# Kernel optimization log

Hardware: AMD Instinct MI355X
Metric: run time of the kernel (lower is better)

Reference implementation:

```python
import jax, jax.numpy as jnp
import numpy as np

N = 100000
DIM = 128
E_A = 500000
E_D = 500000


def setup_inputs() -> dict:
    key = jax.random.key(0)
    ks = jax.random.split(key, 8)
    h = jax.random.normal(ks[0], (N, DIM), dtype=jnp.float32)
    a_idx = jax.random.randint(ks[1], (E_A, 3), 0, N, dtype=jnp.int64 if jax.config.jax_enable_x64 else jnp.int32)
    a_val = jax.random.uniform(ks[2], (E_A, 1), dtype=jnp.float32)
    d_idx = jax.random.randint(ks[3], (E_D, 4), 0, N, dtype=jnp.int64 if jax.config.jax_enable_x64 else jnp.int32)
    d_val = jax.random.uniform(ks[4], (E_D, 1), dtype=jnp.float32)
    # Linear weights stored as [in, out]; init ~ Kaiming-uniform-ish scale
    W_a = jax.random.normal(ks[5], (3 * DIM + 1, DIM), dtype=jnp.float32) * (1.0 / np.sqrt(3 * DIM + 1))
    b_a = jnp.zeros((DIM,), dtype=jnp.float32)
    W_d = jax.random.normal(ks[6], (4 * DIM + 1, DIM), dtype=jnp.float32) * (1.0 / np.sqrt(4 * DIM + 1))
    b_d = jnp.zeros((DIM,), dtype=jnp.float32)
    W_h = jax.random.normal(ks[7], (3 * DIM, DIM), dtype=jnp.float32) * (1.0 / np.sqrt(3 * DIM))
    b_h = jnp.zeros((DIM,), dtype=jnp.float32)
    return {"h": h, "a_idx": a_idx, "a_val": a_val, "d_idx": d_idx, "d_val": d_val,
            "W_a": W_a, "b_a": b_a, "W_d": W_d, "b_d": b_d, "W_h": W_h, "b_h": b_h}


def reference(h, a_idx, a_val, d_idx, d_val, W_a, b_a, W_d, b_d, W_h, b_h):
    n = h.shape[0]
    # angle messages: gather 3 node embeddings + scalar, Linear + SiLU, scatter to center node
    x_a = jnp.concatenate([h[a_idx[:, 0]], h[a_idx[:, 1]], h[a_idx[:, 2]], a_val], axis=-1)  # [E_a, 3d+1]
    m_ijk = jax.nn.silu(x_a @ W_a + b_a)  # [E_a, d]
    agg_a = jax.ops.segment_sum(m_ijk, a_idx[:, 1], num_segments=n)  # [N, d]
    # dihedral messages: gather 4 node embeddings + scalar
    x_d = jnp.concatenate([h[d_idx[:, 0]], h[d_idx[:, 1]], h[d_idx[:, 2]], h[d_idx[:, 3]], d_val], axis=-1)  # [E_d, 4d+1]
    m_ijkl = jax.nn.silu(x_d @ W_d + b_d)  # [E_d, d]
    agg_d = jax.ops.segment_sum(m_ijkl, d_idx[:, 1], num_segments=n)  # [N, d]
    # residual node update
    return h + jnp.concatenate([h, agg_a, agg_d], axis=-1) @ W_h + b_h
```

## Files before the change

kernel.cpp:

```cpp
#include <hip/hip_runtime.h>
#include <hip/hip_bf16.h>

#define DIM 128
#define LDS_STRIDE 136
#define SC_STRIDE 132

typedef __attribute__((ext_vector_type(8))) __bf16 bf16x8;
typedef __attribute__((ext_vector_type(4))) __bf16 bf16x4;
typedef __attribute__((ext_vector_type(4))) float f32x4;


__global__ __launch_bounds__(256) void prep_w(const float* __restrict__ W_a,
                                              const float* __restrict__ W_d,
                                              const float* __restrict__ W_h,
                                              __bf16* __restrict__ Wt)
{
    int idx = blockIdx.x * 256 + threadIdx.x;
    if (idx >= 10 * 16384) return;
    int t   = idx >> 14;
    int rem = idx & 16383;
    int c   = rem >> 7;
    int k   = rem & 127;
    const float* src;
    if (t < 4)      src = W_d + (size_t)t * 16384;
    else if (t < 7) src = W_a + (size_t)(t - 4) * 16384;
    else            src = W_h + (size_t)(t - 7) * 16384;
    Wt[(size_t)t * 16384 + c * 128 + k] = (__bf16)src[k * 128 + c];
}

__global__ __launch_bounds__(256) void count_h2bf(const int* __restrict__ a_idx,
                                                  const int* __restrict__ d_idx,
                                                  int* __restrict__ offs,
                                                  const float* __restrict__ h,
                                                  __bf16* __restrict__ hb,
                                                  int EA, int ED, int N)
{
    const int gt = blockIdx.x * 256 + threadIdx.x;
    if (gt < EA) {
        atomicAdd(&offs[a_idx[3 * (size_t)gt + 1]], 1);
    } else if (gt < EA + ED) {
        int k = gt - EA;
        atomicAdd(&offs[N + d_idx[4 * (size_t)k + 1]], 1);
    }
    int i = gt * 8;
    if (i < N * DIM) {
        float4 v0 = *(const float4*)(h + i);
        float4 v1 = *(const float4*)(h + i + 4);
        bf16x8 o;
        o[0] = (__bf16)v0.x; o[1] = (__bf16)v0.y; o[2] = (__bf16)v0.z; o[3] = (__bf16)v0.w;
        o[4] = (__bf16)v1.x; o[5] = (__bf16)v1.y; o[6] = (__bf16)v1.z; o[7] = (__bf16)v1.w;
        *(bf16x8*)(hb + i) = o;
    }
}

__device__ __forceinline__ void stage_wt(const __bf16* __restrict__ Wtj,
                                         __bf16 (*sB)[LDS_STRIDE], int tid)
{
    for (int it = 0; it < 8; ++it) {
        int idx = tid + it * 256;
        int c  = idx >> 4;
        int k8 = (idx & 15) << 3;
        *(bf16x8*)&sB[c][k8] = *(const bf16x8*)(Wtj + c * 128 + k8);
    }
}

__device__ __forceinline__ void load_afrag_bf16(const __bf16* __restrict__ src,
                                                int row, int stride, int lk, int N,
                                                bf16x8 afrag[4])
{
    const __bf16* rp = src + (size_t)row * stride;
    #pragma unroll
    for (int ks = 0; ks < 4; ++ks) {
        bf16x8 a = {};
        if (row < N) a = *(const bf16x8*)(rp + ks * 32 + lk);
        afrag[ks] = a;
    }
}

__device__ __forceinline__ void proj_body(const __bf16* __restrict__ src,
                                          const __bf16* __restrict__ Wtj,
                                          __bf16* __restrict__ dj,
                                          __bf16 (*sB)[LDS_STRIDE],
                                          int node0, int tid, int N)
{
    float* sC = reinterpret_cast<float*>(sB);
    const int wave = tid >> 6, lane = tid & 63;
    const int lrow = lane & 15;
    const int lk   = (lane >> 4) * 8;
    const int arow = node0 + wave * 16 + lrow;

    stage_wt(Wtj, sB, tid);
    bf16x8 afrag[4];
    load_afrag_bf16(src, arow, DIM, lk, N, afrag);
    __syncthreads();

    f32x4 acc[8];
    #pragma unroll
    for (int ct = 0; ct < 8; ++ct) acc[ct] = (f32x4){0.f, 0.f, 0.f, 0.f};

    #pragma unroll
    for (int ks = 0; ks < 4; ++ks) {
        int k0 = ks * 32 + lk;
        #pragma unroll
        for (int ct = 0; ct < 8; ++ct) {
            bf16x8 b = *(const bf16x8*)&sB[ct * 16 + lrow][k0];
            acc[ct] = __builtin_amdgcn_mfma_f32_16x16x32_bf16(afrag[ks], b, acc[ct], 0, 0, 0);
        }
    }

    __syncthreads();
    {
        int rbase = wave * 16 + (lane >> 4) * 4;
        #pragma unroll
        for (int r = 0; r < 4; ++r)
            #pragma unroll
            for (int ct = 0; ct < 8; ++ct)
                sC[(rbase + r) * SC_STRIDE + ct * 16 + lrow] = acc[ct][r];
    }
    __syncthreads();

    for (int it = 0; it < 8; ++it) {
        int idx = tid + it * 256;
        int row = idx >> 5;
        int c4  = (idx & 31) << 2;
        int grow = node0 + row;
        if (grow < N) {
            const float* sp = sC + row * SC_STRIDE + c4;
            bf16x4 o;
            o[0] = (__bf16)sp[0]; o[1] = (__bf16)sp[1];
            o[2] = (__bf16)sp[2]; o[3] = (__bf16)sp[3];
            *(bf16x4*)(dj + (size_t)grow * DIM + c4) = o;
        }
    }
}

__global__ __launch_bounds__(256, 4) void projD_fill(const int* __restrict__ a_idx,
                                                     const float* __restrict__ a_val,
                                                     const int* __restrict__ d_idx,
                                                     const float* __restrict__ d_val,
                                                     int* __restrict__ offs,
                                                     int4* __restrict__ recs,
                                                     const __bf16* __restrict__ hb,
                                                     const __bf16* __restrict__ Wt,
                                                     __bf16* __restrict__ P,
                                                     int EA, int ED, int N)
{
    __shared__ __bf16 sB[128][LDS_STRIDE];
    const int tid = threadIdx.x;
    const int pb = blockIdx.x;

    int e = pb * 256 + tid;
    if (e < EA) {
        int i0 = a_idx[3 * (size_t)e + 0];
        int i1 = a_idx[3 * (size_t)e + 1];
        int i2 = a_idx[3 * (size_t)e + 2];
        int slot = atomicAdd(&offs[i1], 1);
        recs[slot] = make_int4(i0 * 256, i2 * 256, __float_as_int(a_val[e]), 0);
    } else if (e < EA + ED) {
        int k = e - EA;
        int i0 = d_idx[4 * (size_t)k + 0];
        int i1 = d_idx[4 * (size_t)k + 1];
        int i2 = d_idx[4 * (size_t)k + 2];
        int i3 = d_idx[4 * (size_t)k + 3];
        int slot = atomicAdd(&offs[N + i1], 1);
        recs[slot] = make_int4(i0 * 256, i2 * 256, i3 * 256, __float_as_int(d_val[k]));
    }

    int tile = pb >> 2, j = pb & 3;
    proj_body(hb, Wt + (size_t)j * 16384, P + (size_t)j * N * DIM,
              sB, tile * 64, tid, N);
}

__global__ __launch_bounds__(256, 4) void proj(const __bf16* __restrict__ src,
                                               const __bf16* __restrict__ Wt,
                                               __bf16* __restrict__ dst,
                                               int N)
{
    __shared__ __bf16 sB[128][LDS_STRIDE];
    const int pb = blockIdx.x;
    const int tile = pb >> 2, j = pb & 3;
    proj_body(src, Wt + (size_t)j * 16384, dst + (size_t)j * N * DIM,
              sB, tile * 64, threadIdx.x, N);
}

#define SCAN_CHUNK 1024

__global__ __launch_bounds__(256) void scan_s1(int* __restrict__ data,
                                               int* __restrict__ partials, int n)
{
    __shared__ int lds[256];
    const int t = threadIdx.x;
    const int base = blockIdx.x * SCAN_CHUNK + t * 4;
    int v[4];
    #pragma unroll
    for (int i = 0; i < 4; ++i) v[i] = (base + i < n) ? data[base + i] : 0;
    int tsum = v[0] + v[1] + v[2] + v[3];
    lds[t] = tsum; __syncthreads();
    for (int off = 1; off < 256; off <<= 1) {
        int x = (t >= off) ? lds[t - off] : 0;
        __syncthreads();
        lds[t] += x;
        __syncthreads();
    }
    if (t == 255) partials[blockIdx.x] = lds[255];
    int run = lds[t] - tsum;
    #pragma unroll
    for (int i = 0; i < 4; ++i) {
        int nv = run; run += v[i];
        if (base + i < n) data[base + i] = nv;
    }
}

__global__ __launch_bounds__(256) void scan_s2(int* __restrict__ partials, int nb)
{
    __shared__ int lds[256];
    const int t = threadIdx.x;
    int v = (t < nb) ? partials[t] : 0;
    lds[t] = v; __syncthreads();
    for (int off = 1; off < 256; off <<= 1) {
        int x = (t >= off) ? lds[t - off] : 0;
        __syncthreads();
        lds[t] += x;
        __syncthreads();
    }
    if (t < nb) partials[t] = lds[t] - v;
}

__global__ __launch_bounds__(256) void scan_s3(int* __restrict__ data,
                                               const int* __restrict__ partials, int n)
{
    const int add = partials[blockIdx.x];
    const int base = blockIdx.x * SCAN_CHUNK + threadIdx.x * 4;
    #pragma unroll
    for (int i = 0; i < 4; ++i)
        if (base + i < n) data[base + i] += add;
}

__device__ __forceinline__ float silu(float x)
{
    return x * __builtin_amdgcn_rcpf(1.f + __expf(-x));
}

__global__ __launch_bounds__(256) void gather3(const __bf16* __restrict__ P,
                                               const float* __restrict__ wlast,
                                               const float* __restrict__ bias,
                                               const int* __restrict__ offs,
                                               const int4* __restrict__ recs,
                                               __bf16* __restrict__ aggb, int N)
{
    const int tid = threadIdx.x;
    const int n = blockIdx.x * 4 + (tid >> 6);
    if (n >= N) return;
    const int lane = tid & 63;
    const int half = lane >> 5;
    const int gl = lane & 31;
    const int f  = gl * 4;
    const int fb = gl * 8;
    const size_t NBb = (size_t)N * DIM * 2;
    const char* P0b = (const char*)P;
    const char* P1b = P0b + NBb;
    const char* P2b = P0b + 2 * NBb;
    int start = (n == 0) ? 0 : offs[n - 1];
    int end = offs[n];

    float wl[4], base[4];
    {
        const float* wp = wlast + f;
        const float* bp = bias + f;
        bf16x4 p1 = *(const bf16x4*)(P1b + (size_t)n * 256 + fb);
        #pragma unroll
        for (int c = 0; c < 4; ++c) { wl[c] = wp[c]; base[c] = (float)p1[c] + bp[c]; }
    }
    float a[4] = {0.f, 0.f, 0.f, 0.f};

    const int cnt = end - start;
    const int npair = cnt >> 1;
    int s = start;
    for (int p = 0; p < npair; ++p, s += 2) {
        int4 r = recs[s + half];
        bf16x4 q0 = *(const bf16x4*)(P0b + r.x + fb);
        bf16x4 q2 = *(const bf16x4*)(P2b + r.y + fb);
        float v = __int_as_float(r.z);
        #pragma unroll
        for (int c = 0; c < 4; ++c)
            a[c] += silu((float)q0[c] + (float)q2[c] + v * wl[c] + base[c]);
    }
    if (cnt & 1) {
        int4 r = recs[end - 1];
        bf16x4 q0 = *(const bf16x4*)(P0b + r.x + fb);
        bf16x4 q2 = *(const bf16x4*)(P2b + r.y + fb);
        float v = __int_as_float(r.z);
        if (half == 0) {
            #pragma unroll
            for (int c = 0; c < 4; ++c)
                a[c] += silu((float)q0[c] + (float)q2[c] + v * wl[c] + base[c]);
        }
    }
    #pragma unroll
    for (int c = 0; c < 4; ++c) a[c] += __shfl_xor(a[c], 32, 64);
    if (half == 0) {
        bf16x4 o;
        #pragma unroll
        for (int c = 0; c < 4; ++c) o[c] = (__bf16)a[c];
        *(bf16x4*)(aggb + (size_t)n * 256 + f) = o;
    }
}

__global__ __launch_bounds__(256) void gather4(const __bf16* __restrict__ P,
                                               const float* __restrict__ wlast,
                                               const float* __restrict__ bias,
                                               const int* __restrict__ offs_d,
                                               const int4* __restrict__ recs,
                                               __bf16* __restrict__ agg, int N)
{
    const int tid = threadIdx.x;
    const int n = blockIdx.x * 4 + (tid >> 6);
    if (n >= N) return;
    const int lane = tid & 63;
    const int half = lane >> 5;
    const int gl = lane & 31;
    const int f  = gl * 4;
    const int fb = gl * 8;
    const size_t NBb = (size_t)N * DIM * 2;
    const char* P0b = (const char*)P;
    const char* P1b = P0b + NBb;
    const char* P2b = P0b + 2 * NBb;
    const char* P3b = P0b + 3 * NBb;
    int start = offs_d[n - 1];
    int end = offs_d[n];

    float wl[4], base[4];
    {
        const float* wp = wlast + f;
        const float* bp = bias + f;
        bf16x4 p1 = *(const bf16x4*)(P1b + (size_t)n * 256 + fb);
        #pragma unroll
        for (int c = 0; c < 4; ++c) { wl[c] = wp[c]; base[c] = (float)p1[c] + bp[c]; }
    }
    float a[4] = {0.f, 0.f, 0.f, 0.f};

    const int cnt = end - start;
    const int npair = cnt >> 1;
    int s = start;
    for (int p = 0; p < npair; ++p, s += 2) {
        int4 r = recs[s + half];
        bf16x4 q0 = *(const bf16x4*)(P0b + r.x + fb);
        bf16x4 q2 = *(const bf16x4*)(P2b + r.y + fb);
        bf16x4 q3 = *(const bf16x4*)(P3b + r.z + fb);
        float v = __int_as_float(r.w);
        #pragma unroll
        for (int c = 0; c < 4; ++c)
            a[c] += silu((float)q0[c] + (float)q2[c] + (float)q3[c] + v * wl[c] + base[c]);
    }
    if (cnt & 1) {
        int4 r = recs[end - 1];
        bf16x4 q0 = *(const bf16x4*)(P0b + r.x + fb);
        bf16x4 q2 = *(const bf16x4*)(P2b + r.y + fb);
        bf16x4 q3 = *(const bf16x4*)(P3b + r.z + fb);
        float v = __int_as_float(r.w);
        if (half == 0) {
            #pragma unroll
            for (int c = 0; c < 4; ++c)
                a[c] += silu((float)q0[c] + (float)q2[c] + (float)q3[c] + v * wl[c] + base[c]);
        }
    }
    #pragma unroll
    for (int c = 0; c < 4; ++c) a[c] += __shfl_xor(a[c], 32, 64);
    if (half == 0) {
        bf16x4 o;
        #pragma unroll
        for (int c = 0; c < 4; ++c) o[c] = (__bf16)a[c];
        *(bf16x4*)(agg + (size_t)n * DIM + f) = o;
    }
}

__global__ __launch_bounds__(256, 4) void update2(const float* __restrict__ h,
                                                  const __bf16* __restrict__ aggA,
                                                  const __bf16* __restrict__ aggD,
                                                  const __bf16* __restrict__ PH,
                                                  const __bf16* __restrict__ Wt,
                                                  const float* __restrict__ bh,
                                                  float* __restrict__ out, int N)
{
    __shared__ __bf16 sB[128][LDS_STRIDE];
    float* sC = reinterpret_cast<float*>(sB);
    const int tid = threadIdx.x;
    const int node0 = blockIdx.x * 64;
    const int wave = tid >> 6, lane = tid & 63;
    const int lrow = lane & 15;
    const int lk   = (lane >> 4) * 8;
    const int arow = node0 + wave * 16 + lrow;

    bf16x8 aA[4], aD[4];
    load_afrag_bf16(aggA, arow, 256, lk, N, aA);
    load_afrag_bf16(aggD, arow, DIM, lk, N, aD);

    f32x4 acc[8];
    #pragma unroll
    for (int ct = 0; ct < 8; ++ct) acc[ct] = (f32x4){0.f, 0.f, 0.f, 0.f};

    #pragma unroll
    for (int s = 0; s < 2; ++s) {
        __syncthreads();
        stage_wt(Wt + (size_t)s * 16384, sB, tid);
        __syncthreads();

        #pragma unroll
        for (int ks = 0; ks < 4; ++ks) {
            int k0 = ks * 32 + lk;
            #pragma unroll
            for (int ct = 0; ct < 8; ++ct) {
                bf16x8 b = *(const bf16x8*)&sB[ct * 16 + lrow][k0];
                bf16x8 af = (s == 0) ? aA[ks] : aD[ks];
                acc[ct] = __builtin_amdgcn_mfma_f32_16x16x32_bf16(af, b, acc[ct], 0, 0, 0);
            }
        }
    }

    __syncthreads();
    {
        int rbase = wave * 16 + (lane >> 4) * 4;
        #pragma unroll
        for (int r = 0; r < 4; ++r)
            #pragma unroll
            for (int ct = 0; ct < 8; ++ct)
                sC[(rbase + r) * SC_STRIDE + ct * 16 + lrow] = acc[ct][r];
    }
    __syncthreads();

    for (int it = 0; it < 8; ++it) {
        int idx = tid + it * 256;
        int row = idx >> 5;
        int c4  = (idx & 31) << 2;
        int grow = node0 + row;
        if (grow < N) {
            const float* sp = sC + row * SC_STRIDE + c4;
            float4 rv = *(const float4*)(h + (size_t)grow * DIM + c4);
            float4 bv = *(const float4*)(bh + c4);
            bf16x4 pv = *(const bf16x4*)(PH + (size_t)grow * DIM + c4);
            float4 ov;
            ov.x = rv.x + bv.x + (float)pv[0] + sp[0];
            ov.y = rv.y + bv.y + (float)pv[1] + sp[1];
            ov.z = rv.z + bv.z + (float)pv[2] + sp[2];
            ov.w = rv.w + bv.w + (float)pv[3] + sp[3];
            *(float4*)(out + (size_t)grow * DIM + c4) = ov;
        }
    }
}

static inline size_t align16(size_t x) { return (x + 15) & ~(size_t)15; }

extern "C" void kernel_launch(void* const* d_in, const int* in_sizes, int n_in,
                              void* d_out, int out_size, void* d_ws, size_t ws_size,
                              hipStream_t stream)
{
    const float* h     = (const float*)d_in[0];
    const int*   a_idx = (const int*)d_in[1];
    const float* a_val = (const float*)d_in[2];
    const int*   d_idx = (const int*)d_in[3];
    const float* d_val = (const float*)d_in[4];
    const float* W_a   = (const float*)d_in[5];
    const float* b_a   = (const float*)d_in[6];
    const float* W_d   = (const float*)d_in[7];
    const float* b_d   = (const float*)d_in[8];
    const float* W_h   = (const float*)d_in[9];
    const float* b_h   = (const float*)d_in[10];
    float* out = (float*)d_out;

    const int N  = in_sizes[0] / DIM;
    const int EA = in_sizes[2];
    const int ED = in_sizes[4];
    const size_t NB = (size_t)N * DIM;
    const int twoN = 2 * N;
    const int NBLK = (twoN + SCAN_CHUNK - 1) / SCAN_CHUNK;

    size_t off = 0;
    __bf16* P    = (__bf16*)((char*)d_ws + off); off = align16(off + 4 * NB * sizeof(__bf16));
    __bf16* aggD = (__bf16*)((char*)d_ws + off); off = align16(off + NB * sizeof(__bf16));
    int* offs     = (int*)((char*)d_ws + off);  off = align16(off + (size_t)twoN * sizeof(int));
    int* partials = (int*)((char*)d_ws + off);  off = align16(off + 256 * sizeof(int));
    int4* recs    = (int4*)((char*)d_ws + off); off = align16(off + (size_t)(EA + ED) * sizeof(int4));
    __bf16* Wt  = (__bf16*)((char*)d_ws + off); off = align16(off + (size_t)10 * 16384 * sizeof(__bf16));
    if (ws_size < off) return;

    const int NT64 = (N + 63) / 64;
    const int HB = (int)((NB / 8 + 255) / 256);
    const int GN4 = (N + 3) / 4;

    __bf16* h_bf = (__bf16*)d_out;
    __bf16* aggA = (__bf16*)d_out;

    prep_w<<<(10 * 16384 + 255) / 256, 256, 0, stream>>>(W_a, W_d, W_h, Wt);
    hipMemsetAsync(offs, 0, (size_t)twoN * sizeof(int), stream);

    count_h2bf<<<HB, 256, 0, stream>>>(a_idx, d_idx, offs, h, h_bf, EA, ED, N);

    scan_s1<<<NBLK, 256, 0, stream>>>(offs, partials, twoN);
    scan_s2<<<1, 256, 0, stream>>>(partials, NBLK);
    scan_s3<<<NBLK, 256, 0, stream>>>(offs, partials, twoN);

    projD_fill<<<NT64 * 4, 256, 0, stream>>>(a_idx, a_val, d_idx, d_val,
                                             offs, recs, h_bf, Wt, P, EA, ED, N);

    gather4<<<GN4, 256, 0, stream>>>(P, W_d + 512 * DIM, b_d, offs + N, recs, aggD, N);

    proj<<<NT64 * 4, 256, 0, stream>>>(h_bf, Wt + (size_t)4 * 16384, P, N);

    gather3<<<GN4, 256, 0, stream>>>(P, W_a + 384 * DIM, b_a, offs, recs, aggA, N);

    update2<<<NT64, 256, 0, stream>>>(h, aggA, aggD, P + 3 * NB, Wt + (size_t)8 * 16384,
                                      b_h, out, N);
}
```

Baseline: 319.7 us.

## Co-schedule dihedral gather with angle projection in one interleaved launch

Merges the memory-bound gather4 kernel and the MFMA-based angle projection into a single launch. Every fourth block of the first 4*NPROJ does a projection tile and the rest do gather work, so compute-heavy and latency-bound blocks share the GPU at the same time. The projection writes into a separate workspace buffer so it does not overwrite the dihedral projections gather4 is still reading. This costs extra workspace, uses the projection's LDS footprint and launch bounds for gather blocks as well, and falls back to the old sequence when the workspace is too small.

After: 380.8 us. 1.19x slower.

```diff
diff --git a/kernel.cpp b/kernel.cpp
--- a/kernel.cpp
+++ b/kernel.cpp
@@ -131,6 +131,79 @@
             o[2] = (__bf16)sp[2]; o[3] = (__bf16)sp[3];
             *(bf16x4*)(dj + (size_t)grow * DIM + c4) = o;
         }
+    }
+}
+
+__device__ __forceinline__ float silu(float x)
+{
+    return x * __builtin_amdgcn_rcpf(1.f + __expf(-x));
+}
+
+__device__ __forceinline__ void gather4_body(const __bf16* __restrict__ P,
+                                             const float* __restrict__ wlast,
+                                             const float* __restrict__ bias,
+                                             const int* __restrict__ offs_d,
+                                             const int4* __restrict__ recs,
+                                             __bf16* __restrict__ agg, int N,
+                                             int gid, int tid)
+{
+    const int n = gid * 4 + (tid >> 6);
+    if (n >= N) return;
+    const int lane = tid & 63;
+    const int half = lane >> 5;
+    const int gl = lane & 31;
+    const int f  = gl * 4;
+    const int fb = gl * 8;
+    const size_t NBb = (size_t)N * DIM * 2;
+    const char* P0b = (const char*)P;
+    const char* P1b = P0b + NBb;
+    const char* P2b = P0b + 2 * NBb;
+    const char* P3b = P0b + 3 * NBb;
+    int start = offs_d[n - 1];
+    int end = offs_d[n];
+
+    float wl[4], base[4];
+    {
+        const float* wp = wlast + f;
+        const float* bp = bias + f;
+        bf16x4 p1 = *(const bf16x4*)(P1b + (size_t)n * 256 + fb);
+        #pragma unroll
+        for (int c = 0; c < 4; ++c) { wl[c] = wp[c]; base[c] = (float)p1[c] + bp[c]; }
+    }
+    float a[4] = {0.f, 0.f, 0.f, 0.f};
+
+    const int cnt = end - start;
+    const int npair = cnt >> 1;
+    int s = start;
+    for (int p = 0; p < npair; ++p, s += 2) {
+        int4 r = recs[s + half];
+        bf16x4 q0 = *(const bf16x4*)(P0b + r.x + fb);
+        bf16x4 q2 = *(const bf16x4*)(P2b + r.y + fb);
+        bf16x4 q3 = *(const bf16x4*)(P3b + r.z + fb);
+        float v = __int_as_float(r.w);
+        #pragma unroll
+        for (int c = 0; c < 4; ++c)
+            a[c] += silu((float)q0[c] + (float)q2[c] + (float)q3[c] + v * wl[c] + base[c]);
+    }
+    if (cnt & 1) {
+        int4 r = recs[end - 1];
+        bf16x4 q0 = *(const bf16x4*)(P0b + r.x + fb);
+        bf16x4 q2 = *(const bf16x4*)(P2b + r.y + fb);
+        bf16x4 q3 = *(const bf16x4*)(P3b + r.z + fb);
+        float v = __int_as_float(r.w);
+        if (half == 0) {
+            #pragma unroll
+            for (int c = 0; c < 4; ++c)
+                a[c] += silu((float)q0[c] + (float)q2[c] + (float)q3[c] + v * wl[c] + base[c]);
+        }
+    }
+    #pragma unroll
+    for (int c = 0; c < 4; ++c) a[c] += __shfl_xor(a[c], 32, 64);
+    if (half == 0) {
+        bf16x4 o;
+        #pragma unroll
+        for (int c = 0; c < 4; ++c) o[c] = (__bf16)a[c];
+        *(bf16x4*)(agg + (size_t)n * DIM + f) = o;
     }
 }
 
@@ -183,6 +256,41 @@
               sB, tile * 64, threadIdx.x, N);
 }
 
+__global__ __launch_bounds__(256) void gather4(const __bf16* __restrict__ P,
+                                               const float* __restrict__ wlast,
+                                               const float* __restrict__ bias,
+                                               const int* __restrict__ offs_d,
+                                               const int4* __restrict__ recs,
+                                               __bf16* __restrict__ agg, int N)
+{
+    gather4_body(P, wlast, bias, offs_d, recs, agg, N, blockIdx.x, threadIdx.x);
+}
+
+__global__ __launch_bounds__(256, 4) void ga4_projA(const __bf16* __restrict__ P_dih,
+                                                    const float* __restrict__ wld,
+                                                    const float* __restrict__ bd,
+                                                    const int* __restrict__ offs_d,
+                                                    const int4* __restrict__ recs,
+                                                    __bf16* __restrict__ aggD,
+                                                    const __bf16* __restrict__ hb,
+                                                    const __bf16* __restrict__ Wt4,
+                                                    __bf16* __restrict__ P_ang,
+                                                    int N, int NPROJ)
+{
+    __shared__ __bf16 sB[128][LDS_STRIDE];
+    const int bid = blockIdx.x;
+    const int tid = threadIdx.x;
+    const int pid = bid >> 2, rem = bid & 3;
+    if (rem == 2 && pid < NPROJ) {
+        int tile = pid >> 2, j = pid & 3;
+        proj_body(hb, Wt4 + (size_t)j * 16384, P_ang + (size_t)j * N * DIM,
+                  sB, tile * 64, tid, N);
+    } else {
+        int gid = (pid < NPROJ) ? (bid - pid - (rem > 2 ? 1 : 0)) : (bid - NPROJ);
+        gather4_body(P_dih, wld, bd, offs_d, recs, aggD, N, gid, tid);
+    }
+}
+
 #define SCAN_CHUNK 1024
 
 __global__ __launch_bounds__(256) void scan_s1(int* __restrict__ data,
@@ -234,11 +342,6 @@
     #pragma unroll
     for (int i = 0; i < 4; ++i)
         if (base + i < n) data[base + i] += add;
-}
-
-__device__ __forceinline__ float silu(float x)
-{
-    return x * __builtin_amdgcn_rcpf(1.f + __expf(-x));
 }
 
 __global__ __launch_bounds__(256) void gather3(const __bf16* __restrict__ P,
@@ -303,74 +406,6 @@
         #pragma unroll
         for (int c = 0; c < 4; ++c) o[c] = (__bf16)a[c];
         *(bf16x4*)(aggb + (size_t)n * 256 + f) = o;
-    }
-}
-
-__global__ __launch_bounds__(256) void gather4(const __bf16* __restrict__ P,
-                                               const float* __restrict__ wlast,
-                                               const float* __restrict__ bias,
-                                               const int* __restrict__ offs_d,
-                                               const int4* __restrict__ recs,
-                                               __bf16* __restrict__ agg, int N)
-{
-    const int tid = threadIdx.x;
-    const int n = blockIdx.x * 4 + (tid >> 6);
-    if (n >= N) return;
-    const int lane = tid & 63;
-    const int half = lane >> 5;
-    const int gl = lane & 31;
-    const int f  = gl * 4;
-    const int fb = gl * 8;
-    const size_t NBb = (size_t)N * DIM * 2;
-    const char* P0b = (const char*)P;
-    const char* P1b = P0b + NBb;
-    const char* P2b = P0b + 2 * NBb;
-    const char* P3b = P0b + 3 * NBb;
-    int start = offs_d[n - 1];
-    int end = offs_d[n];
-
-    float wl[4], base[4];
-    {
-        const float* wp = wlast + f;
-        const float* bp = bias + f;
-        bf16x4 p1 = *(const bf16x4*)(P1b + (size_t)n * 256 + fb);
-        #pragma unroll
-        for (int c = 0; c < 4; ++c) { wl[c] = wp[c]; base[c] = (float)p1[c] + bp[c]; }
-    }
-    float a[4] = {0.f, 0.f, 0.f, 0.f};
-
-    const int cnt = end - start;
-    const int npair = cnt >> 1;
-    int s = start;
-    for (int p = 0; p < npair; ++p, s += 2) {
-        int4 r = recs[s + half];
-        bf16x4 q0 = *(const bf16x4*)(P0b + r.x + fb);
-        bf16x4 q2 = *(const bf16x4*)(P2b + r.y + fb);
-        bf16x4 q3 = *(const bf16x4*)(P3b + r.z + fb);
-        float v = __int_as_float(r.w);
-        #pragma unroll
-        for (int c = 0; c < 4; ++c)
-            a[c] += silu((float)q0[c] + (float)q2[c] + (float)q3[c] + v * wl[c] + base[c]);
-    }
-    if (cnt & 1) {
-        int4 r = recs[end - 1];
-        bf16x4 q0 = *(const bf16x4*)(P0b + r.x + fb);
-        bf16x4 q2 = *(const bf16x4*)(P2b + r.y + fb);
-        bf16x4 q3 = *(const bf16x4*)(P3b + r.z + fb);
-        float v = __int_as_float(r.w);
-        if (half == 0) {
-            #pragma unroll
-            for (int c = 0; c < 4; ++c)
-                a[c] += silu((float)q0[c] + (float)q2[c] + (float)q3[c] + v * wl[c] + base[c]);
-        }
-    }
-    #pragma unroll
-    for (int c = 0; c < 4; ++c) a[c] += __shfl_xor(a[c], 32, 64);
-    if (half == 0) {
-        bf16x4 o;
-        #pragma unroll
-        for (int c = 0; c < 4; ++c) o[c] = (__bf16)a[c];
-        *(bf16x4*)(agg + (size_t)n * DIM + f) = o;
     }
 }
 
@@ -483,7 +518,13 @@
     __bf16* Wt  = (__bf16*)((char*)d_ws + off); off = align16(off + (size_t)10 * 16384 * sizeof(__bf16));
     if (ws_size < off) return;
 
+    size_t off_big = off;
+    __bf16* P_ang = (__bf16*)((char*)d_ws + off_big);
+    off_big = align16(off_big + 4 * NB * sizeof(__bf16));
+    const bool BIG = (ws_size >= off_big);
+
     const int NT64 = (N + 63) / 64;
+    const int NPROJ = NT64 * 4;
     const int HB = (int)((NB / 8 + 255) / 256);
     const int GN4 = (N + 3) / 4;
 
@@ -499,15 +540,24 @@
     scan_s2<<<1, 256, 0, stream>>>(partials, NBLK);
     scan_s3<<<NBLK, 256, 0, stream>>>(offs, partials, twoN);
 
-    projD_fill<<<NT64 * 4, 256, 0, stream>>>(a_idx, a_val, d_idx, d_val,
-                                             offs, recs, h_bf, Wt, P, EA, ED, N);
-
-    gather4<<<GN4, 256, 0, stream>>>(P, W_d + 512 * DIM, b_d, offs + N, recs, aggD, N);
-
-    proj<<<NT64 * 4, 256, 0, stream>>>(h_bf, Wt + (size_t)4 * 16384, P, N);
-
-    gather3<<<GN4, 256, 0, stream>>>(P, W_a + 384 * DIM, b_a, offs, recs, aggA, N);
-
-    update2<<<NT64, 256, 0, stream>>>(h, aggA, aggD, P + 3 * NB, Wt + (size_t)8 * 16384,
-                                      b_h, out, N);
-}
+    projD_fill<<<NPROJ, 256, 0, stream>>>(a_idx, a_val, d_idx, d_val,
+                                          offs, recs, h_bf, Wt, P, EA, ED, N);
+
+    const __bf16* Pang_used;
+    if (BIG) {
+        ga4_projA<<<GN4 + NPROJ, 256, 0, stream>>>(P, W_d + 512 * DIM, b_d,
+                                                   offs + N, recs, aggD,
+                                                   h_bf, Wt + (size_t)4 * 16384,
+                                                   P_ang, N, NPROJ);
+        Pang_used = P_ang;
+    } else {
+        gather4<<<GN4, 256, 0, stream>>>(P, W_d + 512 * DIM, b_d, offs + N, recs, aggD, N);
+        proj<<<NPROJ, 256, 0, stream>>>(h_bf, Wt + (size_t)4 * 16384, P, N);
+        Pang_used = P;
+    }
+
+    gather3<<<GN4, 256, 0, stream>>>(Pang_used, W_a + 384 * DIM, b_a, offs, recs, aggA, N);
+
+    update2<<<NT64, 256, 0, stream>>>(h, aggA, aggD, Pang_used + 3 * NB,
+                                      Wt + (size_t)8 * 16384, b_h, out, N);
+}
```

## Fuse all eight projections and both gathers when workspace allows

Applied to the files above, without the earlier changes.

When the workspace has room for a second projection buffer, the dihedral and angle projections (8 weight slices) are computed in one kernel that also fills the edge records. The dihedral and angle gathers then run in one kernel, one node per wavefront. This removes two kernel launches and the serial dependency between projection and gather phases, and lets the gathers share offset loads. It costs an extra 4·N·DIM bf16 workspace buffer and keeps the old path as a fallback.

Result: slower. 333.8 us (+4.4%).

```diff
diff --git a/kernel.cpp b/kernel.cpp
--- a/kernel.cpp
+++ b/kernel.cpp
@@ -134,22 +134,19 @@
     }
 }
 
-__global__ __launch_bounds__(256, 4) void projD_fill(const int* __restrict__ a_idx,
-                                                     const float* __restrict__ a_val,
-                                                     const int* __restrict__ d_idx,
-                                                     const float* __restrict__ d_val,
-                                                     int* __restrict__ offs,
-                                                     int4* __restrict__ recs,
-                                                     const __bf16* __restrict__ hb,
-                                                     const __bf16* __restrict__ Wt,
-                                                     __bf16* __restrict__ P,
-                                                     int EA, int ED, int N)
-{
-    __shared__ __bf16 sB[128][LDS_STRIDE];
-    const int tid = threadIdx.x;
-    const int pb = blockIdx.x;
-
-    int e = pb * 256 + tid;
+__device__ __forceinline__ float silu(float x)
+{
+    return x * __builtin_amdgcn_rcpf(1.f + __expf(-x));
+}
+
+__device__ __forceinline__ void fill_one(const int* __restrict__ a_idx,
+                                         const float* __restrict__ a_val,
+                                         const int* __restrict__ d_idx,
+                                         const float* __restrict__ d_val,
+                                         int* __restrict__ offs,
+                                         int4* __restrict__ recs,
+                                         int e, int EA, int ED, int N)
+{
     if (e < EA) {
         int i0 = a_idx[3 * (size_t)e + 0];
         int i1 = a_idx[3 * (size_t)e + 1];
@@ -165,7 +162,47 @@
         int slot = atomicAdd(&offs[N + i1], 1);
         recs[slot] = make_int4(i0 * 256, i2 * 256, i3 * 256, __float_as_int(d_val[k]));
     }
-
+}
+
+__global__ __launch_bounds__(256, 4) void proj_all_fill(const int* __restrict__ a_idx,
+                                                        const float* __restrict__ a_val,
+                                                        const int* __restrict__ d_idx,
+                                                        const float* __restrict__ d_val,
+                                                        int* __restrict__ offs,
+                                                        int4* __restrict__ recs,
+                                                        const __bf16* __restrict__ hb,
+                                                        const __bf16* __restrict__ Wt,
+                                                        __bf16* __restrict__ P_dih,
+                                                        __bf16* __restrict__ P_ang,
+                                                        int EA, int ED, int N)
+{
+    __shared__ __bf16 sB[128][LDS_STRIDE];
+    const int tid = threadIdx.x;
+    const int pb = blockIdx.x;
+
+    fill_one(a_idx, a_val, d_idx, d_val, offs, recs, pb * 256 + tid, EA, ED, N);
+
+    int tile = pb >> 3, jj = pb & 7;
+    __bf16* dst = (jj < 4) ? P_dih + (size_t)jj * N * DIM
+                           : P_ang + (size_t)(jj - 4) * N * DIM;
+    proj_body(hb, Wt + (size_t)jj * 16384, dst, sB, tile * 64, tid, N);
+}
+
+__global__ __launch_bounds__(256, 4) void projD_fill(const int* __restrict__ a_idx,
+                                                     const float* __restrict__ a_val,
+                                                     const int* __restrict__ d_idx,
+                                                     const float* __restrict__ d_val,
+                                                     int* __restrict__ offs,
+                                                     int4* __restrict__ recs,
+                                                     const __bf16* __restrict__ hb,
+                                                     const __bf16* __restrict__ Wt,
+                                                     __bf16* __restrict__ P,
+                                                     int EA, int ED, int N)
+{
+    __shared__ __bf16 sB[128][LDS_STRIDE];
+    const int tid = threadIdx.x;
+    const int pb = blockIdx.x;
+    fill_one(a_idx, a_val, d_idx, d_val, offs, recs, pb * 256 + tid, EA, ED, N);
     int tile = pb >> 2, j = pb & 3;
     proj_body(hb, Wt + (size_t)j * 16384, P + (size_t)j * N * DIM,
               sB, tile * 64, tid, N);
@@ -236,17 +273,16 @@
         if (base + i < n) data[base + i] += add;
 }
 
-__device__ __forceinline__ float silu(float x)
-{
-    return x * __builtin_amdgcn_rcpf(1.f + __expf(-x));
-}
-
-__global__ __launch_bounds__(256) void gather3(const __bf16* __restrict__ P,
-                                               const float* __restrict__ wlast,
-                                               const float* __restrict__ bias,
-                                               const int* __restrict__ offs,
-                                               const int4* __restrict__ recs,
-                                               __bf16* __restrict__ aggb, int N)
+__global__ __launch_bounds__(256) void gather_both(const __bf16* __restrict__ P_dih,
+                                                   const __bf16* __restrict__ P_ang,
+                                                   const float* __restrict__ wld,
+                                                   const float* __restrict__ bd,
+                                                   const float* __restrict__ wla,
+                                                   const float* __restrict__ ba,
+                                                   const int* __restrict__ offs,
+                                                   const int4* __restrict__ recs,
+                                                   __bf16* __restrict__ aggD,
+                                                   __bf16* __restrict__ aggA, int N)
 {
     const int tid = threadIdx.x;
     const int n = blockIdx.x * 4 + (tid >> 6);
@@ -257,52 +293,107 @@
     const int f  = gl * 4;
     const int fb = gl * 8;
     const size_t NBb = (size_t)N * DIM * 2;
-    const char* P0b = (const char*)P;
-    const char* P1b = P0b + NBb;
-    const char* P2b = P0b + 2 * NBb;
-    int start = (n == 0) ? 0 : offs[n - 1];
-    int end = offs[n];
-
-    float wl[4], base[4];
+
     {
-        const float* wp = wlast + f;
-        const float* bp = bias + f;
-        bf16x4 p1 = *(const bf16x4*)(P1b + (size_t)n * 256 + fb);
-        #pragma unroll
-        for (int c = 0; c < 4; ++c) { wl[c] = wp[c]; base[c] = (float)p1[c] + bp[c]; }
-    }
-    float a[4] = {0.f, 0.f, 0.f, 0.f};
-
-    const int cnt = end - start;
-    const int npair = cnt >> 1;
-    int s = start;
-    for (int p = 0; p < npair; ++p, s += 2) {
-        int4 r = recs[s + half];
-        bf16x4 q0 = *(const bf16x4*)(P0b + r.x + fb);
-        bf16x4 q2 = *(const bf16x4*)(P2b + r.y + fb);
-        float v = __int_as_float(r.z);
-        #pragma unroll
-        for (int c = 0; c < 4; ++c)
-            a[c] += silu((float)q0[c] + (float)q2[c] + v * wl[c] + base[c]);
-    }
-    if (cnt & 1) {
-        int4 r = recs[end - 1];
-        bf16x4 q0 = *(const bf16x4*)(P0b + r.x + fb);
-        bf16x4 q2 = *(const bf16x4*)(P2b + r.y + fb);
-        float v = __int_as_float(r.z);
+        const char* P0b = (const char*)P_dih;
+        const char* P1b = P0b + NBb;
+        const char* P2b = P0b + 2 * NBb;
+        const char* P3b = P0b + 3 * NBb;
+        const int* offs_d = offs + N;
+        int start = offs_d[n - 1];
+        int end = offs_d[n];
+
+        float wl[4], base[4];
+        {
+            const float* wp = wld + f;
+            const float* bp = bd + f;
+            bf16x4 p1 = *(const bf16x4*)(P1b + (size_t)n * 256 + fb);
+            #pragma unroll
+            for (int c = 0; c < 4; ++c) { wl[c] = wp[c]; base[c] = (float)p1[c] + bp[c]; }
+        }
+        float a[4] = {0.f, 0.f, 0.f, 0.f};
+        const int cnt = end - start;
+        const int npair = cnt >> 1;
+        int s = start;
+        for (int p = 0; p < npair; ++p, s += 2) {
+            int4 r = recs[s + half];
+            bf16x4 q0 = *(const bf16x4*)(P0b + r.x + fb);
+            bf16x4 q2 = *(const bf16x4*)(P2b + r.y + fb);
+            bf16x4 q3 = *(const bf16x4*)(P3b + r.z + fb);
+            float v = __int_as_float(r.w);
+            #pragma unroll
+            for (int c = 0; c < 4; ++c)
+                a[c] += silu((float)q0[c] + (float)q2[c] + (float)q3[c] + v * wl[c] + base[c]);
+        }
+        if (cnt & 1) {
+            int4 r = recs[end - 1];
+            bf16x4 q0 = *(const bf16x4*)(P0b + r.x + fb);
+            bf16x4 q2 = *(const bf16x4*)(P2b + r.y + fb);
+            bf16x4 q3 = *(const bf16x4*)(P3b + r.z + fb);
+            float v = __int_as_float(r.w);
+            if (half == 0) {
+                #pragma unroll
+                for (int c = 0; c < 4; ++c)
+                    a[c] += silu((float)q0[c] + (float)q2[c] + (float)q3[c] + v * wl[c] + base[c]);
+            }
+        }
+        #pragma unroll
+        for (int c = 0; c < 4; ++c) a[c] += __shfl_xor(a[c], 32, 64);
         if (half == 0) {
+            bf16x4 o;
+            #pragma unroll
+            for (int c = 0; c < 4; ++c) o[c] = (__bf16)a[c];
+            *(bf16x4*)(aggD + (size_t)n * DIM + f) = o;
+        }
+    }
+
+    {
+        const char* P0b = (const char*)P_ang;
+        const char* P1b = P0b + NBb;
+        const char* P2b = P0b + 2 * NBb;
+        int start = (n == 0) ? 0 : offs[n - 1];
+        int end = offs[n];
+
+        float wl[4], base[4];
+        {
+            const float* wp = wla + f;
+            const float* bp = ba + f;
+            bf16x4 p1 = *(const bf16x4*)(P1b + (size_t)n * 256 + fb);
+            #pragma unroll
+            for (int c = 0; c < 4; ++c) { wl[c] = wp[c]; base[c] = (float)p1[c] + bp[c]; }
+        }
+        float a[4] = {0.f, 0.f, 0.f, 0.f};
+        const int cnt = end - start;
+        const int npair = cnt >> 1;
+        int s = start;
+        for (int p = 0; p < npair; ++p, s += 2) {
+            int4 r = recs[s + half];
+            bf16x4 q0 = *(const bf16x4*)(P0b + r.x + fb);
+            bf16x4 q2 = *(const bf16x4*)(P2b + r.y + fb);
+            float v = __int_as_float(r.z);
             #pragma unroll
             for (int c = 0; c < 4; ++c)
                 a[c] += silu((float)q0[c] + (float)q2[c] + v * wl[c] + base[c]);
         }
-    }
-    #pragma unroll
-    for (int c = 0; c < 4; ++c) a[c] += __shfl_xor(a[c], 32, 64);
-    if (half == 0) {
-        bf16x4 o;
-        #pragma unroll
-        for (int c = 0; c < 4; ++c) o[c] = (__bf16)a[c];
-        *(bf16x4*)(aggb + (size_t)n * 256 + f) = o;
+        if (cnt & 1) {
+            int4 r = recs[end - 1];
+            bf16x4 q0 = *(const bf16x4*)(P0b + r.x + fb);
+            bf16x4 q2 = *(const bf16x4*)(P2b + r.y + fb);
+            float v = __int_as_float(r.z);
+            if (half == 0) {
+                #pragma unroll
+                for (int c = 0; c < 4; ++c)
+                    a[c] += silu((float)q0[c] + (float)q2[c] + v * wl[c] + base[c]);
+            }
+        }
+        #pragma unroll
+        for (int c = 0; c < 4; ++c) a[c] += __shfl_xor(a[c], 32, 64);
+        if (half == 0) {
+            bf16x4 o;
+            #pragma unroll
+            for (int c = 0; c < 4; ++c) o[c] = (__bf16)a[c];
+            *(bf16x4*)(aggA + (size_t)n * 256 + f) = o;
+        }
     }
 }
 
@@ -328,7 +419,6 @@
     const char* P3b = P0b + 3 * NBb;
     int start = offs_d[n - 1];
     int end = offs_d[n];
-
     float wl[4], base[4];
     {
         const float* wp = wlast + f;
@@ -338,7 +428,6 @@
         for (int c = 0; c < 4; ++c) { wl[c] = wp[c]; base[c] = (float)p1[c] + bp[c]; }
     }
     float a[4] = {0.f, 0.f, 0.f, 0.f};
-
     const int cnt = end - start;
     const int npair = cnt >> 1;
     int s = start;
@@ -371,6 +460,69 @@
         #pragma unroll
         for (int c = 0; c < 4; ++c) o[c] = (__bf16)a[c];
         *(bf16x4*)(agg + (size_t)n * DIM + f) = o;
+    }
+}
+
+__global__ __launch_bounds__(256) void gather3(const __bf16* __restrict__ P,
+                                               const float* __restrict__ wlast,
+                                               const float* __restrict__ bias,
+                                               const int* __restrict__ offs,
+                                               const int4* __restrict__ recs,
+                                               __bf16* __restrict__ aggb, int N)
+{
+    const int tid = threadIdx.x;
+    const int n = blockIdx.x * 4 + (tid >> 6);
+    if (n >= N) return;
+    const int lane = tid & 63;
+    const int half = lane >> 5;
+    const int gl = lane & 31;
+    const int f  = gl * 4;
+    const int fb = gl * 8;
+    const size_t NBb = (size_t)N * DIM * 2;
+    const char* P0b = (const char*)P;
+    const char* P1b = P0b + NBb;
+    const char* P2b = P0b + 2 * NBb;
+    int start = (n == 0) ? 0 : offs[n - 1];
+    int end = offs[n];
+    float wl[4], base[4];
+    {
+        const float* wp = wlast + f;
+        const float* bp = bias + f;
+        bf16x4 p1 = *(const bf16x4*)(P1b + (size_t)n * 256 + fb);
+        #pragma unroll
+        for (int c = 0; c < 4; ++c) { wl[c] = wp[c]; base[c] = (float)p1[c] + bp[c]; }
+    }
+    float a[4] = {0.f, 0.f, 0.f, 0.f};
+    const int cnt = end - start;
+    const int npair = cnt >> 1;
+    int s = start;
+    for (int p = 0; p < npair; ++p, s += 2) {
+        int4 r = recs[s + half];
+        bf16x4 q0 = *(const bf16x4*)(P0b + r.x + fb);
+        bf16x4 q2 = *(const bf16x4*)(P2b + r.y + fb);
+        float v = __int_as_float(r.z);
+        #pragma unroll
+        for (int c = 0; c < 4; ++c)
+            a[c] += silu((float)q0[c] + (float)q2[c] + v * wl[c] + base[c]);
+    }
+    if (cnt & 1) {
+        int4 r = recs[end - 1];
+        bf16x4 q0 = *(const bf16x4*)(P0b + r.x + fb);
+        bf16x4 q2 = *(const bf16x4*)(P2b + r.y + fb);
+        float v = __int_as_float(r.z);
+        if (half == 0) {
+            #pragma unroll
+            for (int c = 0; c < 4; ++c)
+                a[c] += silu((float)q0[c] + (float)q2[c] + v * wl[c] + base[c]);
+        }
+    }
+    #pragma unroll
+    for (int c = 0; c < 4; ++c) a[c] += __shfl_xor(a[c], 32, 64);
+    if (half == 0) {
+        bf16x4 o;
+        #pragma unroll
+        for (int c = 0; c < 4; ++c) o[c] = (__bf16)a[c];
+        *(bf16x4*)(aggb + (size_t)n * 256 + f) = o;
     }
 }
 
@@ -483,6 +635,11 @@
     __bf16* Wt  = (__bf16*)((char*)d_ws + off); off = align16(off + (size_t)10 * 16384 * sizeof(__bf16));
     if (ws_size < off) return;
 
+    size_t off_big = off;
+    __bf16* P_ang = (__bf16*)((char*)d_ws + off_big);
+    off_big = align16(off_big + 4 * NB * sizeof(__bf16));
+    const bool BIG = (ws_size >= off_big);
+
     const int NT64 = (N + 63) / 64;
     const int HB = (int)((NB / 8 + 255) / 256);
     const int GN4 = (N + 3) / 4;
@@ -499,15 +656,23 @@
     scan_s2<<<1, 256, 0, stream>>>(partials, NBLK);
     scan_s3<<<NBLK, 256, 0, stream>>>(offs, partials, twoN);
 
-    projD_fill<<<NT64 * 4, 256, 0, stream>>>(a_idx, a_val, d_idx, d_val,
-                                             offs, recs, h_bf, Wt, P, EA, ED, N);
-
-    gather4<<<GN4, 256, 0, stream>>>(P, W_d + 512 * DIM, b_d, offs + N, recs, aggD, N);
-
-    proj<<<NT64 * 4, 256, 0, stream>>>(h_bf, Wt + (size_t)4 * 16384, P, N);
-
-    gather3<<<GN4, 256, 0, stream>>>(P, W_a + 384 * DIM, b_a, offs, recs, aggA, N);
-
-    update2<<<NT64, 256, 0, stream>>>(h, aggA, aggD, P + 3 * NB, Wt + (size_t)8 * 16384,
-                                      b_h, out, N);
-}
+    if (BIG) {
+        proj_all_fill<<<NT64 * 8, 256, 0, stream>>>(a_idx, a_val, d_idx, d_val,
+                                                    offs, recs, h_bf, Wt,
+                                                    P, P_ang, EA, ED, N);
+        gather_both<<<GN4, 256, 0, stream>>>(P, P_ang,
+                                             W_d + 512 * DIM, b_d,
+                                             W_a + 384 * DIM, b_a,
+                                             offs, recs, aggD, aggA, N);
+        update2<<<NT64, 256, 0, stream>>>(h, aggA, aggD, P_ang + 3 * NB,
+                                          Wt + (size_t)8 * 16384, b_h, out, N);
+    } else {
+        projD_fill<<<NT64 * 4, 256, 0, stream>>>(a_idx, a_val, d_idx, d_val,
+                                                 offs, recs, h_bf, Wt, P, EA, ED, N);
+        gather4<<<GN4, 256, 0, stream>>>(P, W_d + 512 * DIM, b_d, offs + N, recs, aggD, N);
+        proj<<<NT64 * 4, 256, 0, stream>>>(h_bf, Wt + (size_t)4 * 16384, P, N);
+        gather3<<<GN4, 256, 0, stream>>>(P, W_a + 384 * DIM, b_a, offs, recs, aggA, N);
+        update2<<<NT64, 256, 0, stream>>>(h, aggA, aggD, P + 3 * NB,
+                                          Wt + (size_t)8 * 16384, b_h, out, N);
+    }
+}
```
